# Performance work log

Measured on AMD Instinct MI355X. Metric: run time of the kernel, lower is better.

The kernel has to match this reference:

```python
import jax, jax.numpy as jnp
import numpy as np

E = 8      # number of experts (sublayers)
N = 8192   # tokens / batch rows
D = 1024   # sublayer input size (max_sublayer_input_size)
H = 2048   # sublayer output size
O = 1024   # output_encoding_size


def setup_inputs() -> dict:
    key = jax.random.key(0)
    k0, k1, k2, k3 = jax.random.split(key, 4)
    x_feat = jax.random.normal(k0, (N, D), dtype=jnp.float32)
    expert_idx = jax.random.randint(k1, (N,), 0, E)  # exclusive (top-1) routing
    # Stacked expert params: sublayers = Linear(D,H), encoders = Linear(H,O)
    W1 = jax.random.normal(k2, (E, D, H), dtype=jnp.float32) * (1.0 / np.sqrt(D))
    b1 = jnp.zeros((E, H), dtype=jnp.float32)
    W2 = jax.random.normal(k3, (E, H, O), dtype=jnp.float32) * (1.0 / np.sqrt(H))
    b2 = jnp.zeros((E, O), dtype=jnp.float32)
    return {"x_feat": x_feat, "W1": W1, "b1": b1, "W2": W2, "b2": b2,
            "expert_idx": expert_idx}


def reference(x_feat, W1, b1, W2, b2, expert_idx):
    # one-hot sublayer_mask (last E columns of the original x)
    onehot = jax.nn.one_hot(expert_idx, E, dtype=x_feat.dtype)  # [N, E]
    # Exclusive dispatch: each token goes through exactly one expert.
    # Structural loop over the fixed E experts; combine via the one-hot mask
    # (equivalent to the original gather -> sublayer -> encoder -> scatter).
    enc = jnp.zeros((x_feat.shape[0], O), dtype=x_feat.dtype)
    for i in range(E):
        h = x_feat @ W1[i] + b1[i]          # [N, H] sublayer
        y = h @ W2[i] + b2[i]               # [N, O] encoder
        enc = enc + onehot[:, i:i + 1] * y  # keep only rows routed to expert i
    # output = [encoded (O cols) | sublayer_mask (E cols)]
    return jnp.concatenate([enc, onehot], axis=1)
```

## Files before the change

### kernel.cpp

```cpp
#include <hip/hip_runtime.h>

#define NTOK 8192
#define DDIM 1024
#define HDIM 2048
#define ODIM 1024
#define NEXP 8
#define OUTW (ODIM + NEXP)
#define MT_MAX 64

typedef __bf16 bf16_t;
typedef bf16_t bf16x8 __attribute__((ext_vector_type(8)));
typedef bf16_t bf16x4 __attribute__((ext_vector_type(4)));
typedef float f32x4 __attribute__((ext_vector_type(4)));

__device__ __forceinline__ void gld_lds16(bf16_t* lds, const bf16_t* g) {
  __builtin_amdgcn_global_load_lds(
      (__attribute__((address_space(1))) void*)g,
      (__attribute__((address_space(3))) void*)lds, 16, 0, 0);
}

__global__ void zero_cnt_kernel(int* cnt) {
  if (threadIdx.x < NEXP) cnt[threadIdx.x] = 0;
}

__global__ void route_kernel(const int* __restrict__ idx, float* __restrict__ out,
                             int* __restrict__ rank, int* cnt) {
  __shared__ int lcnt[NEXP];
  __shared__ int lbase[NEXP];
  int t = threadIdx.x;
  if (t < NEXP) lcnt[t] = 0;
  __syncthreads();
  int n = blockIdx.x * 256 + t;
  int e = idx[n];
  int lr = atomicAdd(&lcnt[e], 1);
  __syncthreads();
  if (t < NEXP) lbase[t] = atomicAdd(&cnt[t], lcnt[t]);
  __syncthreads();
  rank[n] = lbase[e] + lr;
  float* o = out + (size_t)n * OUTW + ODIM;
#pragma unroll
  for (int j = 0; j < NEXP; j++) o[j] = (j == e) ? 1.0f : 0.0f;
}

__global__ void scan_kernel(const int* __restrict__ cnt, int* __restrict__ off) {
  if (threadIdx.x == 0) {
    int s = 0;
    for (int e = 0; e < NEXP; e++) { off[e] = s; s += cnt[e]; }
  }
}

__global__ __launch_bounds__(256) void gather_kernel(
    const float* __restrict__ x, const int* __restrict__ idx,
    const int* __restrict__ rank, const int* __restrict__ off,
    bf16_t* __restrict__ xg, int* __restrict__ tok_of_pos) {
  int wave = threadIdx.x >> 6, lane = threadIdx.x & 63;
  int n = blockIdx.x * 4 + wave;
  int e = idx[n];
  int pos = off[e] + rank[n];
  if (lane == 0) tok_of_pos[pos] = n;
  const float4* xr = (const float4*)(x + (size_t)n * DDIM);
  bf16x4* og = (bf16x4*)(xg + (size_t)pos * DDIM);
#pragma unroll
  for (int r = 0; r < 4; r++) {
    float4 v = xr[lane + r * 64];
    bf16x4 o;
    o[0] = (bf16_t)v.x; o[1] = (bf16_t)v.y; o[2] = (bf16_t)v.z; o[3] = (bf16_t)v.w;
    og[lane + r * 64] = o;
  }
}

__global__ __launch_bounds__(256) void wtrans_kernel(
    const float* __restrict__ W1s, bf16_t* __restrict__ W1d,
    const float* __restrict__ W2s, bf16_t* __restrict__ W2d) {
  __shared__ float t[128][65];
  int id = blockIdx.x;
  const float* src; bf16_t* dst; int R, C, tid2;
  if (id < 2048) { src = W1s; dst = W1d; R = DDIM; C = HDIM; tid2 = id; }
  else           { src = W2s; dst = W2d; R = HDIM; C = ODIM; tid2 = id - 2048; }
  int ntc = C / 64;
  int e = tid2 / (ntc * (R / 128));
  int rem = tid2 % (ntc * (R / 128));
  int c0 = (rem % ntc) * 64, r0g = (rem / ntc) * 128;
  int tid = threadIdx.x;
  const float* s = src + (size_t)e * R * C;
#pragma unroll
  for (int p = 0; p < 8; p++) {
    int r = (tid >> 4) + p * 16;
    int c4 = (tid & 15) * 4;
    float4 v = *(const float4*)&s[(size_t)(r0g + r) * C + c0 + c4];
    t[r][c4 + 0] = v.x;
    t[r][c4 + 1] = v.y;
    t[r][c4 + 2] = v.z;
    t[r][c4 + 3] = v.w;
  }
  __syncthreads();
  bf16_t* d = dst + (size_t)e * R * C;
  int w = tid >> 6, l = tid & 63;
#pragma unroll
  for (int itc = 0; itc < 2; itc++) {
#pragma unroll
    for (int it2 = 0; it2 < 2; it2++) {
      int c = (l >> 3) + 8 * w + 32 * itc;
      int r0 = (l & 7) * 8 + 64 * it2;
      bf16x8 o;
#pragma unroll
      for (int j = 0; j < 8; j++) o[j] = (bf16_t)t[r0 + j][c];
      *(bf16x8*)&d[(size_t)(c0 + c) * R + r0g + r0] = o;
    }
  }
}

template <int KDIM, int NCOLS, int MTG, bool TO_BF16>
__global__ __launch_bounds__(256) void gemm_kernel(
    const bf16_t* __restrict__ A, const bf16_t* __restrict__ Bt,
    const float* __restrict__ bias,
    const int* __restrict__ cnt, const int* __restrict__ off,
    const int* __restrict__ tok_of_pos,
    bf16_t* __restrict__ outb, float* __restrict__ outf) {
  constexpr int NT = NCOLS / 128;
  const int b = blockIdx.x;
  const int e = b & 7;
  int t = b >> 3;
  const int mtl = t % MTG;
  t /= MTG;
  const int nt = t % NT;
  const int g = t / NT;
  const int mt = g * MTG + mtl;

  const int count = cnt[e];
  if (mt * 128 >= count) return;
  const int base = off[e];

  __shared__ bf16_t lA[128 * 64];
  __shared__ bf16_t lB[128 * 64];

  const int tid = threadIdx.x;
  const int lane = tid & 63;
  const int wave = tid >> 6;
  const int mrow = lane & 15;
  const int q = lane >> 4;
  const int wm = (wave & 1) * 64;
  const int wn = (wave >> 1) * 64;

  const bf16_t* pA[4];
  const bf16_t* pB[4];
  const int gchunk = (lane & 7) ^ (lane >> 3);
#pragma unroll
  for (int s = 0; s < 4; s++) {
    int lrow = (wave * 4 + s) * 8 + (lane >> 3);
    int gr = base + mt * 128 + lrow;
    if (gr > NTOK - 1) gr = NTOK - 1;
    pA[s] = A + (size_t)gr * KDIM + gchunk * 8;
    int nrow = nt * 128 + lrow;
    pB[s] = Bt + ((size_t)e * NCOLS + nrow) * KDIM + gchunk * 8;
  }

  f32x4 acc[4][4] = {};
  const int xr = mrow & 7;
  const bf16_t* la0 = &lA[(wm + mrow) * 64];
  const bf16_t* lb0 = &lB[(wn + mrow) * 64];
  const int o0 = (q ^ xr) * 8;
  const int o1 = ((4 + q) ^ xr) * 8;

  for (int kk = 0; kk < KDIM; kk += 64) {
#pragma unroll
    for (int s = 0; s < 4; s++) {
      gld_lds16(&lA[(wave * 4 + s) * 512], pA[s] + kk);
      gld_lds16(&lB[(wave * 4 + s) * 512], pB[s] + kk);
    }
    __syncthreads();
#pragma unroll
    for (int ks = 0; ks < 2; ks++) {
      const int o = ks ? o1 : o0;
      bf16x8 af[4], bfr[4];
#pragma unroll
      for (int i = 0; i < 4; i++) {
        af[i]  = *(const bf16x8*)(la0 + i * 16 * 64 + o);
        bfr[i] = *(const bf16x8*)(lb0 + i * 16 * 64 + o);
      }
#pragma unroll
      for (int i = 0; i < 4; i++)
#pragma unroll
        for (int j = 0; j < 4; j++)
          acc[i][j] = __builtin_amdgcn_mfma_f32_16x16x32_bf16(af[i], bfr[j], acc[i][j], 0, 0, 0);
    }
    __syncthreads();
  }

  const int mlimit = count - mt * 128;
  float bs[4];
#pragma unroll
  for (int j = 0; j < 4; j++)
    bs[j] = bias[(size_t)e * NCOLS + nt * 128 + wn + j * 16 + mrow];

#pragma unroll
  for (int i = 0; i < 4; i++) {
#pragma unroll
    for (int r = 0; r < 4; r++) {
      int ml = wm + i * 16 + q * 4 + r;
      if (ml < mlimit) {
        int prow = base + mt * 128 + ml;
        if constexpr (TO_BF16) {
          bf16_t* orow = outb + (size_t)prow * NCOLS;
#pragma unroll
          for (int j = 0; j < 4; j++)
            orow[nt * 128 + wn + j * 16 + mrow] = (bf16_t)(acc[i][j][r] + bs[j]);
        } else {
          int tok = tok_of_pos[prow];
          float* orow = outf + (size_t)tok * OUTW;
#pragma unroll
          for (int j = 0; j < 4; j++)
            orow[nt * 128 + wn + j * 16 + mrow] = acc[i][j][r] + bs[j];
        }
      }
    }
  }
}

extern "C" void kernel_launch(void* const* d_in, const int* in_sizes, int n_in,
                              void* d_out, int out_size, void* d_ws, size_t ws_size,
                              hipStream_t stream) {
  const float* x  = (const float*)d_in[0];
  const float* W1 = (const float*)d_in[1];
  const float* b1 = (const float*)d_in[2];
  const float* W2 = (const float*)d_in[3];
  const float* b2 = (const float*)d_in[4];
  const int* idx  = (const int*)d_in[5];
  float* out = (float*)d_out;

  char* ws = (char*)d_ws;
  bf16_t* xg  = (bf16_t*)(ws);
  bf16_t* hg  = (bf16_t*)(ws + 16777216);
  bf16_t* Wt1 = (bf16_t*)(ws + 50331648);
  bf16_t* Wt2 = (bf16_t*)(ws + 83886080);
  int* tok    = (int*)(ws + 117440512);
  int* rank   = (int*)(ws + 117473280);
  int* cnt    = (int*)(ws + 117506048);
  int* off    = (int*)(ws + 117506080);

  zero_cnt_kernel<<<1, 64, 0, stream>>>(cnt);
  route_kernel<<<NTOK / 256, 256, 0, stream>>>(idx, out, rank, cnt);
  scan_kernel<<<1, 64, 0, stream>>>(cnt, off);
  gather_kernel<<<NTOK / 4, 256, 0, stream>>>(x, idx, rank, off, xg, tok);
  wtrans_kernel<<<4096, 256, 0, stream>>>(W1, Wt1, W2, Wt2);
  gemm_kernel<DDIM, HDIM, 8, true>
      <<<NEXP * MT_MAX * (HDIM / 128), 256, 0, stream>>>(
      xg, Wt1, b1, cnt, off, tok, hg, nullptr);
  gemm_kernel<HDIM, ODIM, 4, false>
      <<<NEXP * MT_MAX * (ODIM / 128), 256, 0, stream>>>(
      hg, Wt2, b2, cnt, off, tok, nullptr, out);
}
```

Baseline: 328.2 us.

## Enlarge GEMM tiles to 256x128 with K=32 steps and merge prep kernels

The grouped expert GEMMs now use 256-row by 128-column block tiles, with each wave computing 64x128 from a 4x8 MFMA accumulator array. The K step drops from 64 to 32 and the XOR swizzle on LDS is removed, so shared memory per block shrinks. The launch bounds now request two blocks per SM. The token gather and the weight transpose/convert are fused into one prep launch. The aim is more operand reuse per loaded byte and fewer launches, at the cost of higher register pressure, more frequent barriers, and possible LDS bank conflicts without the swizzle.

```diff
diff --git a/kernel.cpp b/kernel.cpp
--- a/kernel.cpp
+++ b/kernel.cpp
@@ -6,7 +6,7 @@
 #define ODIM 1024
 #define NEXP 8
 #define OUTW (ODIM + NEXP)
-#define MT_MAX 64
+#define MT_MAX 32
 
 typedef __bf16 bf16_t;
 typedef bf16_t bf16x8 __attribute__((ext_vector_type(8)));
@@ -49,31 +49,33 @@
   }
 }
 
-__global__ __launch_bounds__(256) void gather_kernel(
+__global__ __launch_bounds__(256) void prep_kernel(
     const float* __restrict__ x, const int* __restrict__ idx,
     const int* __restrict__ rank, const int* __restrict__ off,
-    bf16_t* __restrict__ xg, int* __restrict__ tok_of_pos) {
-  int wave = threadIdx.x >> 6, lane = threadIdx.x & 63;
-  int n = blockIdx.x * 4 + wave;
-  int e = idx[n];
-  int pos = off[e] + rank[n];
-  if (lane == 0) tok_of_pos[pos] = n;
-  const float4* xr = (const float4*)(x + (size_t)n * DDIM);
-  bf16x4* og = (bf16x4*)(xg + (size_t)pos * DDIM);
-#pragma unroll
-  for (int r = 0; r < 4; r++) {
-    float4 v = xr[lane + r * 64];
-    bf16x4 o;
-    o[0] = (bf16_t)v.x; o[1] = (bf16_t)v.y; o[2] = (bf16_t)v.z; o[3] = (bf16_t)v.w;
-    og[lane + r * 64] = o;
-  }
-}
-
-__global__ __launch_bounds__(256) void wtrans_kernel(
+    bf16_t* __restrict__ xg, int* __restrict__ tok_of_pos,
     const float* __restrict__ W1s, bf16_t* __restrict__ W1d,
     const float* __restrict__ W2s, bf16_t* __restrict__ W2d) {
   __shared__ float t[128][65];
   int id = blockIdx.x;
+  int tid = threadIdx.x;
+  if (id < 2048) {
+    int wave = tid >> 6, lane = tid & 63;
+    int n = id * 4 + wave;
+    int e = idx[n];
+    int pos = off[e] + rank[n];
+    if (lane == 0) tok_of_pos[pos] = n;
+    const float4* xr = (const float4*)(x + (size_t)n * DDIM);
+    bf16x4* og = (bf16x4*)(xg + (size_t)pos * DDIM);
+#pragma unroll
+    for (int r = 0; r < 4; r++) {
+      float4 v = xr[lane + r * 64];
+      bf16x4 o;
+      o[0] = (bf16_t)v.x; o[1] = (bf16_t)v.y; o[2] = (bf16_t)v.z; o[3] = (bf16_t)v.w;
+      og[lane + r * 64] = o;
+    }
+    return;
+  }
+  id -= 2048;
   const float* src; bf16_t* dst; int R, C, tid2;
   if (id < 2048) { src = W1s; dst = W1d; R = DDIM; C = HDIM; tid2 = id; }
   else           { src = W2s; dst = W2d; R = HDIM; C = ODIM; tid2 = id - 2048; }
@@ -81,7 +83,6 @@
   int e = tid2 / (ntc * (R / 128));
   int rem = tid2 % (ntc * (R / 128));
   int c0 = (rem % ntc) * 64, r0g = (rem / ntc) * 128;
-  int tid = threadIdx.x;
   const float* s = src + (size_t)e * R * C;
 #pragma unroll
   for (int p = 0; p < 8; p++) {
@@ -111,7 +112,7 @@
 }
 
 template <int KDIM, int NCOLS, int MTG, bool TO_BF16>
-__global__ __launch_bounds__(256) void gemm_kernel(
+__global__ __launch_bounds__(256, 2) void gemm_kernel(
     const bf16_t* __restrict__ A, const bf16_t* __restrict__ Bt,
     const float* __restrict__ bias,
     const int* __restrict__ cnt, const int* __restrict__ off,
@@ -128,70 +129,67 @@
   const int mt = g * MTG + mtl;
 
   const int count = cnt[e];
-  if (mt * 128 >= count) return;
+  if (mt * 256 >= count) return;
   const int base = off[e];
 
-  __shared__ bf16_t lA[128 * 64];
-  __shared__ bf16_t lB[128 * 64];
+  __shared__ bf16_t lA[256 * 32];
+  __shared__ bf16_t lB[128 * 32];
 
   const int tid = threadIdx.x;
   const int lane = tid & 63;
   const int wave = tid >> 6;
   const int mrow = lane & 15;
   const int q = lane >> 4;
-  const int wm = (wave & 1) * 64;
-  const int wn = (wave >> 1) * 64;
+  const int wm = wave * 64;
 
   const bf16_t* pA[4];
-  const bf16_t* pB[4];
-  const int gchunk = (lane & 7) ^ (lane >> 3);
+  const bf16_t* pB[2];
 #pragma unroll
   for (int s = 0; s < 4; s++) {
-    int lrow = (wave * 4 + s) * 8 + (lane >> 3);
-    int gr = base + mt * 128 + lrow;
+    int lrow = (wave * 4 + s) * 16 + (lane >> 2);
+    int gr = base + mt * 256 + lrow;
     if (gr > NTOK - 1) gr = NTOK - 1;
-    pA[s] = A + (size_t)gr * KDIM + gchunk * 8;
+    pA[s] = A + (size_t)gr * KDIM + (lane & 3) * 8;
+  }
+#pragma unroll
+  for (int s = 0; s < 2; s++) {
+    int lrow = (wave * 2 + s) * 16 + (lane >> 2);
     int nrow = nt * 128 + lrow;
-    pB[s] = Bt + ((size_t)e * NCOLS + nrow) * KDIM + gchunk * 8;
-  }
-
-  f32x4 acc[4][4] = {};
-  const int xr = mrow & 7;
-  const bf16_t* la0 = &lA[(wm + mrow) * 64];
-  const bf16_t* lb0 = &lB[(wn + mrow) * 64];
-  const int o0 = (q ^ xr) * 8;
-  const int o1 = ((4 + q) ^ xr) * 8;
-
-  for (int kk = 0; kk < KDIM; kk += 64) {
-#pragma unroll
-    for (int s = 0; s < 4; s++) {
+    pB[s] = Bt + ((size_t)e * NCOLS + nrow) * KDIM + (lane & 3) * 8;
+  }
+
+  f32x4 acc[4][8] = {};
+  const bf16_t* la0 = &lA[(wm + mrow) * 32 + q * 8];
+  const bf16_t* lb0 = &lB[mrow * 32 + q * 8];
+
+  for (int kk = 0; kk < KDIM; kk += 32) {
+#pragma unroll
+    for (int s = 0; s < 4; s++)
       gld_lds16(&lA[(wave * 4 + s) * 512], pA[s] + kk);
-      gld_lds16(&lB[(wave * 4 + s) * 512], pB[s] + kk);
-    }
+#pragma unroll
+    for (int s = 0; s < 2; s++)
+      gld_lds16(&lB[(wave * 2 + s) * 512], pB[s] + kk);
     __syncthreads();
-#pragma unroll
-    for (int ks = 0; ks < 2; ks++) {
-      const int o = ks ? o1 : o0;
-      bf16x8 af[4], bfr[4];
-#pragma unroll
-      for (int i = 0; i < 4; i++) {
-        af[i]  = *(const bf16x8*)(la0 + i * 16 * 64 + o);
-        bfr[i] = *(const bf16x8*)(lb0 + i * 16 * 64 + o);
-      }
-#pragma unroll
-      for (int i = 0; i < 4; i++)
-#pragma unroll
-        for (int j = 0; j < 4; j++)
-          acc[i][j] = __builtin_amdgcn_mfma_f32_16x16x32_bf16(af[i], bfr[j], acc[i][j], 0, 0, 0);
-    }
+    bf16x8 af[4], bfr[8];
+#pragma unroll
+    for (int i = 0; i < 4; i++)
+      af[i] = *(const bf16x8*)(la0 + i * 16 * 32);
+#pragma unroll
+    for (int j = 0; j < 8; j++)
+      bfr[j] = *(const bf16x8*)(lb0 + j * 16 * 32);
+#pragma unroll
+    for (int i = 0; i < 4; i++)
+#pragma unroll
+      for (int j = 0; j < 8; j++)
+        acc[i][j] = __builtin_amdgcn_mfma_f32_16x16x32_bf16(af[i], bfr[j], acc[i][j], 0, 0, 0);
     __syncthreads();
   }
 
-  const int mlimit = count - mt * 128;
-  float bs[4];
-#pragma unroll
-  for (int j = 0; j < 4; j++)
-    bs[j] = bias[(size_t)e * NCOLS + nt * 128 + wn + j * 16 + mrow];
+  const int mlimit = count - mt * 256;
+  float bs[8];
+#pragma unroll
+  for (int j = 0; j < 8; j++)
+    bs[j] = bias[(size_t)e * NCOLS + nt * 128 + j * 16 + mrow];
 
 #pragma unroll
   for (int i = 0; i < 4; i++) {
@@ -199,18 +197,18 @@
     for (int r = 0; r < 4; r++) {
       int ml = wm + i * 16 + q * 4 + r;
       if (ml < mlimit) {
-        int prow = base + mt * 128 + ml;
+        int prow = base + mt * 256 + ml;
         if constexpr (TO_BF16) {
           bf16_t* orow = outb + (size_t)prow * NCOLS;
 #pragma unroll
-          for (int j = 0; j < 4; j++)
-            orow[nt * 128 + wn + j * 16 + mrow] = (bf16_t)(acc[i][j][r] + bs[j]);
+          for (int j = 0; j < 8; j++)
+            orow[nt * 128 + j * 16 + mrow] = (bf16_t)(acc[i][j][r] + bs[j]);
         } else {
           int tok = tok_of_pos[prow];
           float* orow = outf + (size_t)tok * OUTW;
 #pragma unroll
-          for (int j = 0; j < 4; j++)
-            orow[nt * 128 + wn + j * 16 + mrow] = acc[i][j][r] + bs[j];
+          for (int j = 0; j < 8; j++)
+            orow[nt * 128 + j * 16 + mrow] = acc[i][j][r] + bs[j];
         }
       }
     }
@@ -241,12 +239,12 @@
   zero_cnt_kernel<<<1, 64, 0, stream>>>(cnt);
   route_kernel<<<NTOK / 256, 256, 0, stream>>>(idx, out, rank, cnt);
   scan_kernel<<<1, 64, 0, stream>>>(cnt, off);
-  gather_kernel<<<NTOK / 4, 256, 0, stream>>>(x, idx, rank, off, xg, tok);
-  wtrans_kernel<<<4096, 256, 0, stream>>>(W1, Wt1, W2, Wt2);
-  gemm_kernel<DDIM, HDIM, 8, true>
+  prep_kernel<<<6144, 256, 0, stream>>>(x, idx, rank, off, xg, tok,
+                                        W1, Wt1, W2, Wt2);
+  gemm_kernel<DDIM, HDIM, 4, true>
       <<<NEXP * MT_MAX * (HDIM / 128), 256, 0, stream>>>(
       xg, Wt1, b1, cnt, off, tok, hg, nullptr);
-  gemm_kernel<HDIM, ODIM, 4, false>
+  gemm_kernel<HDIM, ODIM, 2, false>
       <<<NEXP * MT_MAX * (ODIM / 128), 256, 0, stream>>>(
       hg, Wt2, b2, cnt, off, tok, nullptr, out);
 }
```

After: 337.1 us. 1.03x slower.
